# Performance work log

Measured on AMD Instinct MI355X. Metric: run time of the kernel, lower is better.

The kernel has to match this reference:

```python
import jax, jax.numpy as jnp
import numpy as np

B_J0 = 0.01
BETA = 1.8
GAMMA = 0.5
LENS = 0.5
TAU_M = 20.0
DT = 1.0
IN_SIZE = 4
FULL_LEN = 784
T_STEPS = FULL_LEN // IN_SIZE  # 196 sequential steps
H1, H2, H3 = 512, 512, 512
OUT = 10
BATCH = 256


@jax.custom_vjp
def spike_fn(x):
    # ActFun_adp: heaviside forward, rectangular surrogate backward
    return (x > 0).astype(x.dtype)

def _spike_fwd(x):
    return (x > 0).astype(x.dtype), x

def _spike_bwd(x, g):
    return (GAMMA * g * (jnp.abs(x) < LENS).astype(g.dtype),)

spike_fn.defvjp(_spike_fwd, _spike_bwd)


def _make_mask(dim, c_min, c_max, min_dc, max_dc, phase_max, T=784):
    # Faithful port of create_general_mask
    dc_steps = np.linspace(min_dc, max_dc, dim)
    cycles = np.linspace(c_min, c_max, dim)
    phases = np.linspace(0.0, float(int(phase_max * c_max)), dim)
    rows = []
    for cyc, dc, ph in zip(cycles, dc_steps, phases):
        cyc = int(np.ceil(cyc))
        on = int(np.ceil(dc * cyc))
        pat = [1] * on + [0] * (cyc - on)
        p = int(np.round(ph))
        if p > 0:
            pat = pat[-p:] + pat[:-p]
        rows.append(pat * (T // cyc) + pat[: T % cyc])
    return jnp.asarray(np.array(rows, dtype=np.float32))


def setup_inputs() -> dict:
    key = jax.random.key(0)
    ks = jax.random.split(key, 8)

    def xav(k, o, i):
        return jax.random.normal(k, (o, i), jnp.float32) * np.float32(np.sqrt(2.0 / (o + i)))

    return {
        "x": jax.random.uniform(ks[0], (BATCH, FULL_LEN), jnp.float32),
        "W_i2h1": xav(ks[1], H1, IN_SIZE), "b_i2h1": jnp.zeros(H1, jnp.float32),
        "W_h2h1": xav(ks[2], H1, H1), "b_h2h1": jnp.zeros(H1, jnp.float32),
        "W_i2h2": xav(ks[3], H2, H1), "b_i2h2": jnp.zeros(H2, jnp.float32),
        "W_h2h2": xav(ks[4], H2, H2), "b_h2h2": jnp.zeros(H2, jnp.float32),
        "W_i2h3": xav(ks[5], H3, H2), "b_i2h3": jnp.zeros(H3, jnp.float32),
        "W_h2o": xav(ks[6], OUT, H3), "b_h2o": jnp.zeros(OUT, jnp.float32),
        "tau_adp_h1": jnp.full((H1,), 700.0, jnp.float32),
        "tau_adp_h2": jnp.full((H2,), 700.0, jnp.float32),
        "tau_adp_h3": jnp.full((H3,), 700.0, jnp.float32),
        "mask1": _make_mask(H1, 2, 10, 0.1, 0.9, 0.5),
        "mask2": _make_mask(H2, 2, 10, 0.1, 0.9, 0.5),
        "mask3": _make_mask(H3, 2, 10, 0.1, 0.9, 0.5),
    }


def _forward(x, params, mask1, mask2, mask3):
    (W_i2h1, b_i2h1, W_h2h1, b_h2h1, W_i2h2, b_i2h2, W_h2h2, b_h2h2,
     W_i2h3, b_i2h3, W_h2o, b_h2o, tau1, tau2, tau3) = params
    N = x.shape[0]
    # Faithful to torch: condition uses self.T (196), not 784, so most steps
    # reuse the last IN_SIZE columns.
    cols = np.stack([
        np.arange(s * IN_SIZE, s * IN_SIZE + IN_SIZE)
        if s * IN_SIZE < T_STEPS - IN_SIZE
        else np.arange(FULL_LEN - IN_SIZE, FULL_LEN)
        for s in range(T_STEPS)
    ])
    x_seq = jnp.transpose(x[:, cols], (1, 0, 2))  # (T, N, IN)
    alpha = jnp.exp(jnp.float32(-DT / TAU_M))
    ro1 = jnp.exp(-DT / tau1)
    ro2 = jnp.exp(-DT / tau2)
    ro3 = jnp.exp(-DT / tau3)
    m1_seq = mask1[:, :T_STEPS].T  # (T, H1)
    m2_seq = mask2[:, :T_STEPS].T
    m3_seq = mask3[:, :T_STEPS].T

    def upd(inputs, mem, spk, ro, b, mask):
        # mem_update_NU_adp_skip, isAdapt=1
        b = ro * b + (1.0 - ro) * spk
        Bth = B_J0 + BETA * b
        new_mem = mem * alpha + (1.0 - alpha) * inputs - Bth * spk * DT
        mem = jnp.where(mask == 0, mem, new_mem)
        spk = spike_fn(mem - Bth) * mask
        return mem, spk, b

    def step(carry, xs):
        mem1, s1, bb1, mem2, s2, bb2, mem3, s3, bb3, acc = carry
        x_t, mk1, mk2, mk3 = xs
        h1 = x_t @ W_i2h1.T + b_i2h1 + s1 @ W_h2h1.T + b_h2h1
        mem1, s1, bb1 = upd(h1, mem1, s1, ro1, bb1, mk1)
        h2 = s1 @ W_i2h2.T + b_i2h2 + s2 @ W_h2h2.T + b_h2h2
        mem2, s2, bb2 = upd(h2, mem2, s2, ro2, bb2, mk2)
        h3 = s2 @ W_i2h3.T + b_i2h3
        mem3, s3, bb3 = upd(h3, mem3, s3, ro3, bb3, mk3)
        acc = acc + s3 @ W_h2o.T + b_h2o
        return (mem1, s1, bb1, mem2, s2, bb2, mem3, s3, bb3, acc), None

    z = lambda h: jnp.zeros((N, h), x.dtype)
    bj = lambda h: jnp.full((N, h), B_J0, x.dtype)  # b starts at scalar b_j0
    carry0 = (z(H1), z(H1), bj(H1), z(H2), z(H2), bj(H2), z(H3), z(H3), bj(H3), z(OUT))
    carry, _ = jax.lax.scan(step, carry0, (x_seq, m1_seq, m2_seq, m3_seq))
    return carry[-1] / T_STEPS


def reference(x, W_i2h1, b_i2h1, W_h2h1, b_h2h1, W_i2h2, b_i2h2, W_h2h2, b_h2h2,
              W_i2h3, b_i2h3, W_h2o, b_h2o, tau_adp_h1, tau_adp_h2, tau_adp_h3,
              mask1, mask2, mask3):
    params = (W_i2h1, b_i2h1, W_h2h1, b_h2h1, W_i2h2, b_i2h2, W_h2h2, b_h2h2,
              W_i2h3, b_i2h3, W_h2o, b_h2o, tau_adp_h1, tau_adp_h2, tau_adp_h3)
    return _forward(x, params, mask1, mask2, mask3)
```

## Files before the change

### kernel.cpp

```cpp
#include <hip/hip_runtime.h>

#define H 512
#define TSTEPS 196
#define FLEN 784
#define NBATCH 256

typedef float f4 __attribute__((ext_vector_type(4)));
typedef unsigned long long ull;

#define MBOFF_F 1048576

__global__ void transpose4(const float* __restrict__ a,
                           const float* __restrict__ b,
                           const float* __restrict__ c,
                           const float* __restrict__ d,
                           float* __restrict__ ws)
{
    __shared__ float tile[32][33];
    const float* src = (blockIdx.z == 0) ? a : (blockIdx.z == 1) ? b
                     : (blockIdx.z == 2) ? c : d;
    float* dst = ws + (size_t)blockIdx.z * (H * H);
    int bx = blockIdx.x * 32, by = blockIdx.y * 32;
    int tx = threadIdx.x, ty = threadIdx.y;
    for (int r = ty; r < 32; r += 8)
        tile[r][tx] = src[(by + r) * H + bx + tx];
    __syncthreads();
    for (int r = ty; r < 32; r += 8)
        dst[(bx + r) * H + by + tx] = tile[tx][r];
}

__global__ void maskbits(const float* __restrict__ m1, const float* __restrict__ m2,
                         const float* __restrict__ m3, ull* __restrict__ mb)
{
    int t = blockIdx.x;
    int z = blockIdx.y;
    int l = threadIdx.x;
    const float* src = (z == 0) ? m1 : (z == 1) ? m2 : m3;
    for (int w = 0; w < 8; ++w) {
        ull bl = __ballot(src[(w * 64 + l) * FLEN + t] != 0.0f);
        if (l == 0) mb[(size_t)z * (TSTEPS * 8) + t * 8 + w] = bl;
    }
}

__device__ __forceinline__ void gpair(const char* __restrict__ bA,
                                      const char* __restrict__ bB,
                                      const unsigned* __restrict__ list,
                                      int lo, int hi, unsigned uoff,
                                      f4& accA, f4& accB)
{
    int i = lo;
    for (; i + 4 <= hi; i += 4) {
        unsigned o0 = list[i]     + uoff;
        unsigned o1 = list[i + 1] + uoff;
        unsigned o2 = list[i + 2] + uoff;
        unsigned o3 = list[i + 3] + uoff;
        f4 va0 = *(const f4*)(bA + o0), vb0 = *(const f4*)(bB + o0);
        f4 va1 = *(const f4*)(bA + o1), vb1 = *(const f4*)(bB + o1);
        f4 va2 = *(const f4*)(bA + o2), vb2 = *(const f4*)(bB + o2);
        f4 va3 = *(const f4*)(bA + o3), vb3 = *(const f4*)(bB + o3);
        accA += (va0 + va1) + (va2 + va3);
        accB += (vb0 + vb1) + (vb2 + vb3);
    }
    for (; i < hi; ++i) {
        unsigned o = list[i] + uoff;
        accA += *(const f4*)(bA + o);
        accB += *(const f4*)(bB + o);
    }
}

__device__ __forceinline__ float sum8(const float* __restrict__ p, int j)
{
    float s0 = p[j] + p[512 + j];
    float s1 = p[1024 + j] + p[1536 + j];
    float s2 = p[2048 + j] + p[2560 + j];
    float s3 = p[3072 + j] + p[3584 + j];
    return (s0 + s1) + (s2 + s3);
}

__device__ __forceinline__ float mbit(const ull* __restrict__ mb, int t, int j)
{
    return ((mb[t * 8 + (j >> 6)] >> (j & 63)) & 1ull) ? 1.0f : 0.0f;
}

__global__ __launch_bounds__(1024)
void lsnn_main(const float* __restrict__ x,
               const float* __restrict__ Wi1,
               const float* __restrict__ bi1, const float* __restrict__ bh1,
               const float* __restrict__ bi2, const float* __restrict__ bh2,
               const float* __restrict__ bi3,
               const float* __restrict__ Wo,  const float* __restrict__ bo,
               const float* __restrict__ tau1, const float* __restrict__ tau2,
               const float* __restrict__ tau3,
               const float* __restrict__ ws,
               float* __restrict__ out)
{
    const char* wsb = (const char*)ws;
    const char* B_H1 = wsb;
    const char* B_I2 = wsb + (1u << 20);
    const char* B_H2 = wsb + (2u << 20);
    const char* B_I3 = wsb + (3u << 20);
    const ull* mb1 = (const ull*)(ws + MBOFF_F);
    const ull* mb2 = mb1 + TSTEPS * 8;
    const ull* mb3 = mb2 + TSTEPS * 8;

    const int n    = blockIdx.x;
    const int tid  = threadIdx.x;
    const int lane = tid & 63;
    const bool lowh = tid < 512;
    const int j    = lowh ? tid : tid - 512;
    const int w8   = (tid >> 6) & 7;
    const int u    = tid & 127;
    const int g    = tid >> 7;
    const unsigned uoff = (unsigned)u << 4;

    __shared__ f4       pU1[8][128], pU2[8][128], pU3[8][128];
    __shared__ unsigned L1[H], L2[H];
    __shared__ ull      ballS[16];

    float4 wi; float bs1, ro1, omr1, mem1, b1, s1;
    float bs2, ro2, omr2, mem2, b2, s2;
    float bs3, ro3, omr3, mem3, b3, s3, cnt3;
    const float alpha = expf(-1.0f / 20.0f);
    const float oma = 1.0f - alpha;
    if (lowh) {
        wi  = reinterpret_cast<const float4*>(Wi1)[j];
        bs1 = bi1[j] + bh1[j];
        ro1 = expf(-1.0f / tau1[j]); omr1 = 1.0f - ro1;
        mem1 = 0.f; b1 = 0.01f; s1 = 0.f;
    } else {
        bs2 = bi2[j] + bh2[j];
        bs3 = bi3[j];
        ro2 = expf(-1.0f / tau2[j]); omr2 = 1.0f - ro2;
        ro3 = expf(-1.0f / tau3[j]); omr3 = 1.0f - ro3;
        mem2 = 0.f; b2 = 0.01f; s2 = 0.f;
        mem3 = 0.f; b3 = 0.01f; s3 = 0.f; cnt3 = 0.f;
    }

    int na1 = 0, na2 = 0;
    const float* xr = x + n * FLEN;

    if (tid < 16) ballS[tid] = 0ull;
    __syncthreads();

    for (int t = 0; t <= TSTEPS + 1; ++t) {
        {
            int tot = na1 + na2;
            int lo = (tot * g) >> 3, hi = (tot * (g + 1)) >> 3;
            f4 aU1 = (f4)0.0f, aU2 = (f4)0.0f, aU3 = (f4)0.0f;
            int mi = lo < na1 ? (hi < na1 ? hi : na1) : na1;
            if (lo < mi)
                gpair(B_H1, B_I2, L1, lo, mi, uoff, aU1, aU2);
            int lo2 = (lo > na1 ? lo : na1) - na1, hi2 = hi - na1;
            if (lo2 < hi2)
                gpair(B_H2, B_I3, L2, lo2, hi2, uoff, aU2, aU3);
            pU1[g][u] = aU1;
            pU2[g][u] = aU2;
            pU3[g][u] = aU3;
        }
        __syncthreads();

        if (lowh) {
            ull ball = 0;
            if (t < TSTEPS) {
                float mk1 = mbit(mb1, t, j);
                int base = (t < 48) ? (4 * t) : (FLEN - 4);
                float4 xv = *reinterpret_cast<const float4*>(xr + base);
                float h1 = wi.x * xv.x + wi.y * xv.y + wi.z * xv.z + wi.w * xv.w
                         + bs1 + sum8((const float*)&pU1[0][0], j);
                b1 = ro1 * b1 + omr1 * s1;
                float Bth = 0.01f + 1.8f * b1;
                float nm = mem1 * alpha + oma * h1 - Bth * s1;
                mem1 = (mk1 == 0.0f) ? mem1 : nm;
                s1 = (mem1 - Bth > 0.0f) ? mk1 : 0.0f;
                ball = __ballot(s1 != 0.0f);
            }
            if (lane == 0) ballS[w8] = ball;
        } else {
            ull ball = 0;
            int t2 = t - 1;
            if (t2 >= 0 && t2 < TSTEPS) {
                float mk2 = mbit(mb2, t2, j);
                float h2 = bs2 + sum8((const float*)&pU2[0][0], j);
                b2 = ro2 * b2 + omr2 * s2;
                float Bth = 0.01f + 1.8f * b2;
                float nm = mem2 * alpha + oma * h2 - Bth * s2;
                mem2 = (mk2 == 0.0f) ? mem2 : nm;
                s2 = (mem2 - Bth > 0.0f) ? mk2 : 0.0f;
                ball = __ballot(s2 != 0.0f);
            }
            if (lane == 0) ballS[8 + w8] = ball;
            int t3 = t - 2;
            if (t3 >= 0 && t3 < TSTEPS) {
                float mk3 = mbit(mb3, t3, j);
                float h3 = bs3 + sum8((const float*)&pU3[0][0], j);
                b3 = ro3 * b3 + omr3 * s3;
                float Bth = 0.01f + 1.8f * b3;
                float nm = mem3 * alpha + oma * h3 - Bth * s3;
                mem3 = (mk3 == 0.0f) ? mem3 : nm;
                s3 = (mem3 - Bth > 0.0f) ? mk3 : 0.0f;
                cnt3 += s3;
            }
        }
        __syncthreads();

        {
            ull bw[16];
            int c[16];
#pragma unroll
            for (int w = 0; w < 16; ++w) { bw[w] = ballS[w]; c[w] = __popcll(bw[w]); }
            int t1 = 0, t2s = 0;
#pragma unroll
            for (int w = 0; w < 8; ++w) { t1 += c[w]; t2s += c[8 + w]; }
            if (lowh) {
                int pos = 0;
#pragma unroll
                for (int w = 0; w < 8; ++w) if (w < w8) pos += c[w];
                pos += __popcll(bw[w8] & ((1ull << lane) - 1ull));
                if ((bw[w8] >> lane) & 1ull) L1[pos] = (unsigned)j << 11;
            } else {
                int pos = 0;
#pragma unroll
                for (int w = 0; w < 8; ++w) if (w < w8) pos += c[8 + w];
                pos += __popcll(bw[8 + w8] & ((1ull << lane) - 1ull));
                if ((bw[8 + w8] >> lane) & 1ull) L2[pos] = (unsigned)j << 11;
            }
            na1 = t1; na2 = t2s;
        }
        __syncthreads();
    }

    float* c3 = (float*)&pU1[0][0];
    if (!lowh) c3[j] = cnt3;
    __syncthreads();
    int wv = tid >> 6;
    for (int o = wv; o < 10; o += 16) {
        float p = 0.0f;
        for (int i = lane; i < H; i += 64)
            p += Wo[o * H + i] * c3[i];
        for (int off = 32; off > 0; off >>= 1)
            p += __shfl_down(p, off);
        if (lane == 0)
            out[n * 10 + o] = (p + 196.0f * bo[o]) / 196.0f;
    }
}

extern "C" void kernel_launch(void* const* d_in, const int* in_sizes, int n_in,
                              void* d_out, int out_size, void* d_ws, size_t ws_size,
                              hipStream_t stream)
{
    const float* x    = (const float*)d_in[0];
    const float* Wi1  = (const float*)d_in[1];
    const float* bi1  = (const float*)d_in[2];
    const float* Wh1  = (const float*)d_in[3];
    const float* bh1  = (const float*)d_in[4];
    const float* Wi2  = (const float*)d_in[5];
    const float* bi2  = (const float*)d_in[6];
    const float* Wh2  = (const float*)d_in[7];
    const float* bh2  = (const float*)d_in[8];
    const float* Wi3  = (const float*)d_in[9];
    const float* bi3  = (const float*)d_in[10];
    const float* Wo   = (const float*)d_in[11];
    const float* bo   = (const float*)d_in[12];
    const float* tau1 = (const float*)d_in[13];
    const float* tau2 = (const float*)d_in[14];
    const float* tau3 = (const float*)d_in[15];
    const float* m1   = (const float*)d_in[16];
    const float* m2   = (const float*)d_in[17];
    const float* m3   = (const float*)d_in[18];

    float* ws  = (float*)d_ws;
    float* out = (float*)d_out;

    transpose4<<<dim3(16, 16, 4), dim3(32, 8, 1), 0, stream>>>(Wh1, Wi2, Wh2, Wi3, ws);
    maskbits<<<dim3(TSTEPS, 3, 1), 64, 0, stream>>>(m1, m2, m3, (ull*)(ws + MBOFF_F));

    lsnn_main<<<NBATCH, 1024, 0, stream>>>(x, Wi1, bi1, bh1, bi2, bh2, bi3,
                                           Wo, bo, tau1, tau2, tau3, ws, out);
}
```

Before: 630.2 us.

## Skip masked-off neuron gathers and pad spike lists with zero row

Each thread group now reads the per-timestep mask nibble for its four output neurons and skips the weight gather for a layer when all four are masked, since their membranes would not update. Spike lists are padded to a multiple of four with an offset pointing at an appended zero row in each weight slot, which removes the remainder loop. The weight slots are enlarged to hold that zero row, and maskbits gets an extra grid slice to zero it. Gathers for layer 2 input and recurrent weights are now separate passes rather than paired loads, which may lose some load overlap.

```diff
diff --git a/kernel.cpp b/kernel.cpp
--- a/kernel.cpp
+++ b/kernel.cpp
@@ -8,7 +8,10 @@
 typedef float f4 __attribute__((ext_vector_type(4)));
 typedef unsigned long long ull;
 
-#define MBOFF_F 1048576
+#define SLOTB  1050624u
+#define SLOTF  262656
+#define PADOFF 1048576u
+#define MBOFF_F 1050624
 
 __global__ void transpose4(const float* __restrict__ a,
                            const float* __restrict__ b,
@@ -19,7 +22,7 @@
     __shared__ float tile[32][33];
     const float* src = (blockIdx.z == 0) ? a : (blockIdx.z == 1) ? b
                      : (blockIdx.z == 2) ? c : d;
-    float* dst = ws + (size_t)blockIdx.z * (H * H);
+    float* dst = ws + (size_t)blockIdx.z * SLOTF;
     int bx = blockIdx.x * 32, by = blockIdx.y * 32;
     int tx = threadIdx.x, ty = threadIdx.y;
     for (int r = ty; r < 32; r += 8)
@@ -30,11 +33,20 @@
 }
 
 __global__ void maskbits(const float* __restrict__ m1, const float* __restrict__ m2,
-                         const float* __restrict__ m3, ull* __restrict__ mb)
+                         const float* __restrict__ m3, float* __restrict__ ws)
 {
     int t = blockIdx.x;
     int z = blockIdx.y;
     int l = threadIdx.x;
+    if (z == 3) {
+        int idx = t * 64 + l;
+        if (idx < 4 * 512) {
+            int slot = idx >> 9, pos = idx & 511;
+            ws[(size_t)slot * SLOTF + 512 * 512 + pos] = 0.0f;
+        }
+        return;
+    }
+    ull* mb = (ull*)(ws + MBOFF_F);
     const float* src = (z == 0) ? m1 : (z == 1) ? m2 : m3;
     for (int w = 0; w < 8; ++w) {
         ull bl = __ballot(src[(w * 64 + l) * FLEN + t] != 0.0f);
@@ -42,30 +54,22 @@
     }
 }
 
-__device__ __forceinline__ void gpair(const char* __restrict__ bA,
-                                      const char* __restrict__ bB,
+__device__ __forceinline__ f4 gsingle(const char* __restrict__ base,
                                       const unsigned* __restrict__ list,
-                                      int lo, int hi, unsigned uoff,
-                                      f4& accA, f4& accB)
-{
-    int i = lo;
-    for (; i + 4 <= hi; i += 4) {
+                                      int lo, int hi, unsigned uoff)
+{
+    f4 a0 = (f4)0.0f, a1 = (f4)0.0f, a2 = (f4)0.0f, a3 = (f4)0.0f;
+    for (int i = lo; i < hi; i += 4) {
         unsigned o0 = list[i]     + uoff;
         unsigned o1 = list[i + 1] + uoff;
         unsigned o2 = list[i + 2] + uoff;
         unsigned o3 = list[i + 3] + uoff;
-        f4 va0 = *(const f4*)(bA + o0), vb0 = *(const f4*)(bB + o0);
-        f4 va1 = *(const f4*)(bA + o1), vb1 = *(const f4*)(bB + o1);
-        f4 va2 = *(const f4*)(bA + o2), vb2 = *(const f4*)(bB + o2);
-        f4 va3 = *(const f4*)(bA + o3), vb3 = *(const f4*)(bB + o3);
-        accA += (va0 + va1) + (va2 + va3);
-        accB += (vb0 + vb1) + (vb2 + vb3);
-    }
-    for (; i < hi; ++i) {
-        unsigned o = list[i] + uoff;
-        accA += *(const f4*)(bA + o);
-        accB += *(const f4*)(bB + o);
-    }
+        a0 += *(const f4*)(base + o0);
+        a1 += *(const f4*)(base + o1);
+        a2 += *(const f4*)(base + o2);
+        a3 += *(const f4*)(base + o3);
+    }
+    return (a0 + a1) + (a2 + a3);
 }
 
 __device__ __forceinline__ float sum8(const float* __restrict__ p, int j)
@@ -94,11 +98,11 @@
                const float* __restrict__ ws,
                float* __restrict__ out)
 {
-    const char* wsb = (const char*)ws;
+    const char* wsb  = (const char*)ws;
     const char* B_H1 = wsb;
-    const char* B_I2 = wsb + (1u << 20);
-    const char* B_H2 = wsb + (2u << 20);
-    const char* B_I3 = wsb + (3u << 20);
+    const char* B_I2 = wsb + SLOTB;
+    const char* B_H2 = wsb + 2 * SLOTB;
+    const char* B_I3 = wsb + 3 * SLOTB;
     const ull* mb1 = (const ull*)(ws + MBOFF_F);
     const ull* mb2 = mb1 + TSTEPS * 8;
     const ull* mb3 = mb2 + TSTEPS * 8;
@@ -136,7 +140,7 @@
         mem3 = 0.f; b3 = 0.01f; s3 = 0.f; cnt3 = 0.f;
     }
 
-    int na1 = 0, na2 = 0;
+    int na1 = 0, na2 = 0, na1p = 0, na2p = 0;
     const float* xr = x + n * FLEN;
 
     if (tid < 16) ballS[tid] = 0ull;
@@ -144,15 +148,24 @@
 
     for (int t = 0; t <= TSTEPS + 1; ++t) {
         {
-            int tot = na1 + na2;
-            int lo = (tot * g) >> 3, hi = (tot * (g + 1)) >> 3;
+            unsigned nib1 = 0, nib2 = 0, nib3 = 0;
+            if (t < TSTEPS)
+                nib1 = (unsigned)((mb1[t * 8 + (u >> 4)] >> ((u & 15) * 4)) & 0xFull);
+            if (t >= 1 && t - 1 < TSTEPS)
+                nib2 = (unsigned)((mb2[(t - 1) * 8 + (u >> 4)] >> ((u & 15) * 4)) & 0xFull);
+            if (t >= 2)
+                nib3 = (unsigned)((mb3[(t - 2) * 8 + (u >> 4)] >> ((u & 15) * 4)) & 0xFull);
+
+            int lo1 = ((na1p * g) >> 3) & ~3, hi1 = ((na1p * (g + 1)) >> 3) & ~3;
+            int lo2 = ((na2p * g) >> 3) & ~3, hi2 = ((na2p * (g + 1)) >> 3) & ~3;
+
             f4 aU1 = (f4)0.0f, aU2 = (f4)0.0f, aU3 = (f4)0.0f;
-            int mi = lo < na1 ? (hi < na1 ? hi : na1) : na1;
-            if (lo < mi)
-                gpair(B_H1, B_I2, L1, lo, mi, uoff, aU1, aU2);
-            int lo2 = (lo > na1 ? lo : na1) - na1, hi2 = hi - na1;
-            if (lo2 < hi2)
-                gpair(B_H2, B_I3, L2, lo2, hi2, uoff, aU2, aU3);
+            if (nib1) aU1 = gsingle(B_H1, L1, lo1, hi1, uoff);
+            if (nib2) {
+                aU2 = gsingle(B_I2, L1, lo1, hi1, uoff);
+                aU2 += gsingle(B_H2, L2, lo2, hi2, uoff);
+            }
+            if (nib3) aU3 = gsingle(B_I3, L2, lo2, hi2, uoff);
             pU1[g][u] = aU1;
             pU2[g][u] = aU2;
             pU3[g][u] = aU3;
@@ -225,6 +238,9 @@
                 if ((bw[8 + w8] >> lane) & 1ull) L2[pos] = (unsigned)j << 11;
             }
             na1 = t1; na2 = t2s;
+            na1p = (na1 + 3) & ~3; na2p = (na2 + 3) & ~3;
+            if (tid < 4)      { if (na1 + tid < na1p) L1[na1 + tid] = PADOFF; }
+            else if (tid < 8) { int q = tid - 4; if (na2 + q < na2p) L2[na2 + q] = PADOFF; }
         }
         __syncthreads();
     }
@@ -272,7 +288,7 @@
     float* out = (float*)d_out;
 
     transpose4<<<dim3(16, 16, 4), dim3(32, 8, 1), 0, stream>>>(Wh1, Wi2, Wh2, Wi3, ws);
-    maskbits<<<dim3(TSTEPS, 3, 1), 64, 0, stream>>>(m1, m2, m3, (ull*)(ws + MBOFF_F));
+    maskbits<<<dim3(TSTEPS, 4, 1), 64, 0, stream>>>(m1, m2, m3, ws);
 
     lsnn_main<<<NBATCH, 1024, 0, stream>>>(x, Wi1, bi1, bh1, bi2, bh2, bi3,
                                            Wo, bo, tau1, tau2, tau3, ws, out);
```

Result: slower. 756.7 us (+20.1%).

## Walk spike ballot bitmasks directly instead of compacting active lists

Applied to the files above, without the earlier changes.

Removes the per-step prefix-sum compaction phase that built shared active-neuron index lists, along with one block-wide barrier per time step. Each pair of waves now reads the ballot words, extracts its own byte slice of spiking neurons into a 64-bit mask, and gathers weight rows by iterating set bits. Groups of four are padded with a zero column that the mask kernel writes, so the inner loop has no remainder. The cost is an uneven load across wave pairs, since work per pair now follows the spike distribution rather than an even split.

```diff
diff --git a/kernel.cpp b/kernel.cpp
--- a/kernel.cpp
+++ b/kernel.cpp
@@ -8,7 +8,11 @@
 typedef float f4 __attribute__((ext_vector_type(4)));
 typedef unsigned long long ull;
 
-#define MBOFF_F 1048576
+#define PAD1 4194304u
+#define PAD2 2097152u
+#define ZCOL1_F 1048576
+#define ZCOL2_F 1310720
+#define MBOFF_F 1311232
 
 __global__ void transpose4(const float* __restrict__ a,
                            const float* __restrict__ b,
@@ -30,11 +34,18 @@
 }
 
 __global__ void maskbits(const float* __restrict__ m1, const float* __restrict__ m2,
-                         const float* __restrict__ m3, ull* __restrict__ mb)
+                         const float* __restrict__ m3, float* __restrict__ ws)
 {
     int t = blockIdx.x;
     int z = blockIdx.y;
     int l = threadIdx.x;
+    if (z == 3) {
+        int idx = t * 64 + l;
+        if (idx < 512)            ws[ZCOL1_F + idx] = 0.0f;
+        else if (idx < 1024)      ws[ZCOL2_F + idx - 512] = 0.0f;
+        return;
+    }
+    ull* mb = (ull*)(ws + MBOFF_F);
     const float* src = (z == 0) ? m1 : (z == 1) ? m2 : m3;
     for (int w = 0; w < 8; ++w) {
         ull bl = __ballot(src[(w * 64 + l) * FLEN + t] != 0.0f);
@@ -42,29 +53,25 @@
     }
 }
 
-__device__ __forceinline__ void gpair(const char* __restrict__ bA,
-                                      const char* __restrict__ bB,
-                                      const unsigned* __restrict__ list,
-                                      int lo, int hi, unsigned uoff,
-                                      f4& accA, f4& accB)
-{
-    int i = lo;
-    for (; i + 4 <= hi; i += 4) {
-        unsigned o0 = list[i]     + uoff;
-        unsigned o1 = list[i + 1] + uoff;
-        unsigned o2 = list[i + 2] + uoff;
-        unsigned o3 = list[i + 3] + uoff;
-        f4 va0 = *(const f4*)(bA + o0), vb0 = *(const f4*)(bB + o0);
-        f4 va1 = *(const f4*)(bA + o1), vb1 = *(const f4*)(bB + o1);
-        f4 va2 = *(const f4*)(bA + o2), vb2 = *(const f4*)(bB + o2);
-        f4 va3 = *(const f4*)(bA + o3), vb3 = *(const f4*)(bB + o3);
+__device__ __forceinline__ void walkpair(const char* __restrict__ bA,
+                                         const char* __restrict__ bB,
+                                         ull comp, unsigned pairi, unsigned padc,
+                                         unsigned uoff, f4& accA, f4& accB)
+{
+    int cnt = __popcll(comp);
+    for (int e = 0; e < cnt; e += 4) {
+        unsigned o0, o1, o2, o3;
+#define EXT(o) { if (comp) { int q = __builtin_ctzll(comp); comp &= comp - 1ull;  \
+                 o = ((((unsigned)q & ~7u) | pairi) << 14) | (((unsigned)q & 7u) << 11); } \
+                 else o = padc; }
+        EXT(o0) EXT(o1) EXT(o2) EXT(o3)
+#undef EXT
+        f4 va0 = *(const f4*)(bA + o0 + uoff), vb0 = *(const f4*)(bB + o0 + uoff);
+        f4 va1 = *(const f4*)(bA + o1 + uoff), vb1 = *(const f4*)(bB + o1 + uoff);
+        f4 va2 = *(const f4*)(bA + o2 + uoff), vb2 = *(const f4*)(bB + o2 + uoff);
+        f4 va3 = *(const f4*)(bA + o3 + uoff), vb3 = *(const f4*)(bB + o3 + uoff);
         accA += (va0 + va1) + (va2 + va3);
         accB += (vb0 + vb1) + (vb2 + vb3);
-    }
-    for (; i < hi; ++i) {
-        unsigned o = list[i] + uoff;
-        accA += *(const f4*)(bA + o);
-        accB += *(const f4*)(bB + o);
     }
 }
 
@@ -94,28 +101,26 @@
                const float* __restrict__ ws,
                float* __restrict__ out)
 {
-    const char* wsb = (const char*)ws;
+    const char* wsb  = (const char*)ws;
     const char* B_H1 = wsb;
-    const char* B_I2 = wsb + (1u << 20);
     const char* B_H2 = wsb + (2u << 20);
-    const char* B_I3 = wsb + (3u << 20);
     const ull* mb1 = (const ull*)(ws + MBOFF_F);
     const ull* mb2 = mb1 + TSTEPS * 8;
     const ull* mb3 = mb2 + TSTEPS * 8;
 
-    const int n    = blockIdx.x;
-    const int tid  = threadIdx.x;
-    const int lane = tid & 63;
+    const int n     = blockIdx.x;
+    const int tid   = threadIdx.x;
+    const int lane  = tid & 63;
+    const int w     = tid >> 6;
+    const unsigned pairi = (unsigned)(w >> 1);
+    const int u     = ((w & 1) << 6) | lane;
+    const unsigned uoff = (unsigned)u << 4;
     const bool lowh = tid < 512;
-    const int j    = lowh ? tid : tid - 512;
-    const int w8   = (tid >> 6) & 7;
-    const int u    = tid & 127;
-    const int g    = tid >> 7;
-    const unsigned uoff = (unsigned)u << 4;
-
-    __shared__ f4       pU1[8][128], pU2[8][128], pU3[8][128];
-    __shared__ unsigned L1[H], L2[H];
-    __shared__ ull      ballS[16];
+    const int j     = lowh ? tid : tid - 512;
+    const int w8    = (tid >> 6) & 7;
+
+    __shared__ f4  pU1[8][128], pU2[8][128], pU3[8][128];
+    __shared__ ull ballS[16];
 
     float4 wi; float bs1, ro1, omr1, mem1, b1, s1;
     float bs2, ro2, omr2, mem2, b2, s2;
@@ -136,26 +141,37 @@
         mem3 = 0.f; b3 = 0.01f; s3 = 0.f; cnt3 = 0.f;
     }
 
-    int na1 = 0, na2 = 0;
     const float* xr = x + n * FLEN;
+    const unsigned shf = (pairi & 3u) * 8u;
 
     if (tid < 16) ballS[tid] = 0ull;
     __syncthreads();
 
     for (int t = 0; t <= TSTEPS + 1; ++t) {
         {
-            int tot = na1 + na2;
-            int lo = (tot * g) >> 3, hi = (tot * (g + 1)) >> 3;
+            unsigned lo1[8], hi1[8], lo2[8], hi2[8];
+#pragma unroll
+            for (int wd = 0; wd < 8; ++wd) {
+                ull v1 = ballS[wd], v2 = ballS[8 + wd];
+                lo1[wd] = __builtin_amdgcn_readfirstlane((unsigned)v1);
+                hi1[wd] = __builtin_amdgcn_readfirstlane((unsigned)(v1 >> 32));
+                lo2[wd] = __builtin_amdgcn_readfirstlane((unsigned)v2);
+                hi2[wd] = __builtin_amdgcn_readfirstlane((unsigned)(v2 >> 32));
+            }
+            ull comp1 = 0ull, comp2 = 0ull;
+#pragma unroll
+            for (int wd = 0; wd < 8; ++wd) {
+                unsigned by1 = ((pairi < 4u ? lo1[wd] : hi1[wd]) >> shf) & 0xFFu;
+                unsigned by2 = ((pairi < 4u ? lo2[wd] : hi2[wd]) >> shf) & 0xFFu;
+                comp1 |= (ull)by1 << (8 * wd);
+                comp2 |= (ull)by2 << (8 * wd);
+            }
             f4 aU1 = (f4)0.0f, aU2 = (f4)0.0f, aU3 = (f4)0.0f;
-            int mi = lo < na1 ? (hi < na1 ? hi : na1) : na1;
-            if (lo < mi)
-                gpair(B_H1, B_I2, L1, lo, mi, uoff, aU1, aU2);
-            int lo2 = (lo > na1 ? lo : na1) - na1, hi2 = hi - na1;
-            if (lo2 < hi2)
-                gpair(B_H2, B_I3, L2, lo2, hi2, uoff, aU2, aU3);
-            pU1[g][u] = aU1;
-            pU2[g][u] = aU2;
-            pU3[g][u] = aU3;
+            walkpair(B_H1, B_H1 + (1u << 20), comp1, pairi, PAD1, uoff, aU1, aU2);
+            walkpair(B_H2, B_H2 + (1u << 20), comp2, pairi, PAD2, uoff, aU2, aU3);
+            pU1[pairi][u] = aU1;
+            pU2[pairi][u] = aU2;
+            pU3[pairi][u] = aU3;
         }
         __syncthreads();
 
@@ -200,31 +216,6 @@
                 s3 = (mem3 - Bth > 0.0f) ? mk3 : 0.0f;
                 cnt3 += s3;
             }
-        }
-        __syncthreads();
-
-        {
-            ull bw[16];
-            int c[16];
-#pragma unroll
-            for (int w = 0; w < 16; ++w) { bw[w] = ballS[w]; c[w] = __popcll(bw[w]); }
-            int t1 = 0, t2s = 0;
-#pragma unroll
-            for (int w = 0; w < 8; ++w) { t1 += c[w]; t2s += c[8 + w]; }
-            if (lowh) {
-                int pos = 0;
-#pragma unroll
-                for (int w = 0; w < 8; ++w) if (w < w8) pos += c[w];
-                pos += __popcll(bw[w8] & ((1ull << lane) - 1ull));
-                if ((bw[w8] >> lane) & 1ull) L1[pos] = (unsigned)j << 11;
-            } else {
-                int pos = 0;
-#pragma unroll
-                for (int w = 0; w < 8; ++w) if (w < w8) pos += c[8 + w];
-                pos += __popcll(bw[8 + w8] & ((1ull << lane) - 1ull));
-                if ((bw[8 + w8] >> lane) & 1ull) L2[pos] = (unsigned)j << 11;
-            }
-            na1 = t1; na2 = t2s;
         }
         __syncthreads();
     }
@@ -272,7 +263,7 @@
     float* out = (float*)d_out;
 
     transpose4<<<dim3(16, 16, 4), dim3(32, 8, 1), 0, stream>>>(Wh1, Wi2, Wh2, Wi3, ws);
-    maskbits<<<dim3(TSTEPS, 3, 1), 64, 0, stream>>>(m1, m2, m3, (ull*)(ws + MBOFF_F));
+    maskbits<<<dim3(TSTEPS, 4, 1), 64, 0, stream>>>(m1, m2, m3, ws);
 
     lsnn_main<<<NBATCH, 1024, 0, stream>>>(x, Wi1, bi1, bh1, bi2, bh2, bi3,
                                            Wo, bo, tau1, tau2, tau3, ws, out);
```

New measurement: 668.4 us. 6.1% more time.
